# Kernel tuning notes

Hardware: AMD Instinct MI355X
Metric: run time of the kernel (lower is better)

The kernel has to match this reference:

```python
import jax, jax.numpy as jnp
import numpy as np

N_NODES = 80000
N_EDGES = 1280000
IN_CH = 128
OUT_CH = 32
HID = 2 * OUT_CH


def gcn_conv(x, W, b, src, dst, n_nodes):
    """PyG GCNConv with self-loops and symmetric normalization.
    out[i] = b + sum_{j->i} deg(j)^-1/2 deg(i)^-1/2 (x_j @ W)
    """
    loop = jnp.arange(n_nodes, dtype=src.dtype)
    s = jnp.concatenate([src, loop])  # [E+N]
    d = jnp.concatenate([dst, loop])  # [E+N]
    deg = jax.ops.segment_sum(jnp.ones_like(d, dtype=x.dtype), d,
                              num_segments=n_nodes)  # in-degree incl. self loop
    dinv = jnp.where(deg > 0, jax.lax.rsqrt(deg), 0.0)
    norm = dinv[s] * dinv[d]  # [E+N]
    h = x @ W  # [N, F_out] dense transform first (fewer flops when F_out < F_in)
    msg = h[s] * norm[:, None]  # [E+N, F_out] gather + scale
    out = jax.ops.segment_sum(msg, d, num_segments=n_nodes)  # scatter-add
    return out + b


def setup_inputs() -> dict:
    key = jax.random.key(0)
    k1, k2, k3, k4 = jax.random.split(key, 4)
    x = jax.random.normal(k1, (N_NODES, IN_CH), dtype=jnp.float32)
    edge_index = jax.random.randint(k2, (2, N_EDGES), 0, N_NODES, dtype=jnp.int64)
    W1 = jax.random.normal(k3, (IN_CH, HID), dtype=jnp.float32) / np.sqrt(IN_CH)
    b1 = jnp.zeros((HID,), dtype=jnp.float32)
    W2 = jax.random.normal(k4, (HID, OUT_CH), dtype=jnp.float32) / np.sqrt(HID)
    b2 = jnp.zeros((OUT_CH,), dtype=jnp.float32)
    return {"x": x, "edge_index": edge_index, "W1": W1, "b1": b1,
            "W2": W2, "b2": b2}


def reference(x, edge_index, W1, b1, W2, b2):
    src, dst = edge_index[0], edge_index[1]
    h = jax.nn.relu(gcn_conv(x, W1, b1, src, dst, N_NODES))
    return gcn_conv(h, W2, b2, src, dst, N_NODES)
```

## Files before the change

### kernel.cpp

```cpp
#include <hip/hip_runtime.h>
#include <hip/hip_fp16.h>

#define N_NODES 80000
#define N_EDGES 1280000
#define IN_CH 128
#define HID 64
#define OUT_CH 32

#define NBUCK 625
#define CAP 3072
#define BIN_BLOCKS 256

typedef float vf2 __attribute__((ext_vector_type(2)));
typedef float vf4 __attribute__((ext_vector_type(4)));
typedef short short8 __attribute__((ext_vector_type(8)));
typedef float floatx4 __attribute__((ext_vector_type(4)));

__device__ __forceinline__ unsigned bf16rn(float x) {
    unsigned u = __float_as_uint(x);
    return (u + 0x7FFFu + ((u >> 16) & 1u)) >> 16;
}
__device__ __forceinline__ unsigned packbf2(float a, float b) {
    return bf16rn(a) | (bf16rn(b) << 16);
}
__device__ __forceinline__ float hl(unsigned u) {
    return __half2float(__ushort_as_half((unsigned short)(u & 0xFFFFu)));
}
__device__ __forceinline__ float hh(unsigned u) {
    return __half2float(__ushort_as_half((unsigned short)(u >> 16)));
}
__device__ __forceinline__ unsigned pack2h(float a, float b) {
    return (unsigned)__half_as_ushort(__float2half_rn(a)) |
           ((unsigned)__half_as_ushort(__float2half_rn(b)) << 16);
}

__global__ __launch_bounds__(256) void k_bin_gemm1(
        const int* __restrict__ src, const int* __restrict__ dst,
        int* __restrict__ gcur, unsigned int* __restrict__ binned,
        const float* __restrict__ x, const float* __restrict__ W1,
        unsigned short* __restrict__ h1h) {
    __shared__ unsigned short smem_u[26112];
    int bid = blockIdx.x, t = threadIdx.x;
    if (bid < BIN_BLOCKS) {
        int* hist = (int*)smem_u;
        int* lcur = hist + NBUCK;
        const int chunk = N_EDGES / BIN_BLOCKS;
        int e0 = bid * chunk;
        int e1 = e0 + chunk;
        for (int i = t; i < NBUCK; i += 256) hist[i] = 0;
        __syncthreads();
        for (int e = e0 + t; e < e1; e += 256)
            atomicAdd(&hist[dst[e] >> 7], 1);
        __syncthreads();
        for (int i = t; i < NBUCK; i += 256) {
            int h = hist[i];
            lcur[i] = h ? atomicAdd(&gcur[i], h) : 0;
        }
        __syncthreads();
        for (int e = e0 + t; e < e1; e += 256) {
            int d = dst[e];
            int bk = d >> 7;
            int pos = atomicAdd(&lcur[bk], 1);
            if (pos < CAP)
                binned[(size_t)bk * CAP + pos] =
                    (unsigned int)src[e] | ((unsigned int)(d & 127) << 17);
        }
    } else {
        unsigned short* sX = smem_u;
        unsigned short* sWT = smem_u + 128 * 136;
        long long nb = (long long)(bid - BIN_BLOCKS) * 128;
        for (int it = 0; it < 16; ++it) {
            int idx = t + it * 256;
            int node = idx >> 5, k4 = (idx & 31) * 4;
            float4 v = *(const float4*)&x[(nb + node) * IN_CH + k4];
            unsigned u0 = packbf2(v.x, v.y), u1 = packbf2(v.z, v.w);
            *(uint2*)&sX[node * 136 + k4] = (uint2){u0, u1};
        }
        for (int it = 0; it < 8; ++it) {
            int idx = t + it * 256;
            int k = idx >> 4, c4 = (idx & 15) * 4;
            float4 w = *(const float4*)&W1[k * 64 + c4];
            sWT[(c4 + 0) * 136 + k] = (unsigned short)bf16rn(w.x);
            sWT[(c4 + 1) * 136 + k] = (unsigned short)bf16rn(w.y);
            sWT[(c4 + 2) * 136 + k] = (unsigned short)bf16rn(w.z);
            sWT[(c4 + 3) * 136 + k] = (unsigned short)bf16rn(w.w);
        }
        __syncthreads();
        int wv = t >> 6, lane = t & 63;
        int lm = lane & 15, q = lane >> 4;
        int m0 = wv * 32;
        floatx4 acc[2][4];
#pragma unroll
        for (int i = 0; i < 2; ++i)
#pragma unroll
            for (int j = 0; j < 4; ++j) acc[i][j] = (floatx4){0.f, 0.f, 0.f, 0.f};
#pragma unroll
        for (int kk = 0; kk < 128; kk += 32) {
            short8 a0 = *(short8*)&sX[(m0 + lm) * 136 + kk + q * 8];
            short8 a1 = *(short8*)&sX[(m0 + 16 + lm) * 136 + kk + q * 8];
#pragma unroll
            for (int ct = 0; ct < 4; ++ct) {
                short8 bfr = *(short8*)&sWT[(ct * 16 + lm) * 136 + kk + q * 8];
                acc[0][ct] = __builtin_amdgcn_mfma_f32_16x16x32_bf16(a0, bfr, acc[0][ct], 0, 0, 0);
                acc[1][ct] = __builtin_amdgcn_mfma_f32_16x16x32_bf16(a1, bfr, acc[1][ct], 0, 0, 0);
            }
        }
#pragma unroll
        for (int mt = 0; mt < 2; ++mt)
#pragma unroll
            for (int ct = 0; ct < 4; ++ct)
#pragma unroll
                for (int r = 0; r < 4; ++r) {
                    long long node = nb + m0 + mt * 16 + q * 4 + r;
                    int c = ct * 16 + lm;
                    h1h[node * 64 + c] = __half_as_ushort(__float2half_rn(acc[mt][ct][r]));
                }
    }
}

__global__ __launch_bounds__(256) void k_csr(const unsigned int* __restrict__ binned,
                                             const int* __restrict__ cnt,
                                             int* __restrict__ csr,
                                             int* __restrict__ rs, int* __restrict__ re,
                                             float* __restrict__ dinv) {
    __shared__ int deg[128];
    __shared__ int scan[128];
    __shared__ int cur[128];
    int bk = blockIdx.x, t = threadIdx.x;
    int n_e = min(cnt[bk], CAP);
    const unsigned int* eb = binned + (size_t)bk * CAP;
    if (t < 128) deg[t] = 0;
    __syncthreads();
    for (int i = t; i < n_e; i += 256) atomicAdd(&deg[eb[i] >> 17], 1);
    __syncthreads();
    if (t < 128) scan[t] = deg[t];
    __syncthreads();
    for (int off = 1; off < 128; off <<= 1) {
        int v = (t < 128 && t >= off) ? scan[t - off] : 0;
        __syncthreads();
        if (t < 128) scan[t] += v;
        __syncthreads();
    }
    if (t < 128) {
        int incl = scan[t];
        int s = incl - deg[t];
        cur[t] = s;
        int n = bk * 128 + t;
        int base = bk * CAP;
        rs[n] = base + s;
        re[n] = base + incl;
        dinv[n] = rsqrtf((float)(deg[t] + 1));
    }
    __syncthreads();
    for (int i = t; i < n_e; i += 256) {
        unsigned int p = eb[i];
        int dL = p >> 17;
        int pos = atomicAdd(&cur[dL], 1);
        csr[bk * CAP + pos] = (int)(p & 0x1FFFF);
    }
}

__global__ __launch_bounds__(256) void k_agg64(
        const unsigned int* __restrict__ h1u, const int* __restrict__ csr,
        const int* __restrict__ rs_, const int* __restrict__ re_,
        const float* __restrict__ dinv, const float* __restrict__ b1,
        float* __restrict__ h2) {
    int n = blockIdx.x * 4 + (threadIdx.x >> 6);
    int lane = threadIdx.x & 63;
    int half = lane >> 5, fo = lane & 31;
    int a = rs_[n], b = re_[n];
    float ax = 0.f, ay = 0.f;
    int e = a + half;
    for (; e + 6 < b; e += 8) {
        int s0 = csr[e], s1 = csr[e + 2], s2 = csr[e + 4], s3 = csr[e + 6];
        unsigned u0 = h1u[(size_t)s0 * 32 + fo]; float d0 = dinv[s0];
        unsigned u1 = h1u[(size_t)s1 * 32 + fo]; float d1 = dinv[s1];
        unsigned u2 = h1u[(size_t)s2 * 32 + fo]; float d2 = dinv[s2];
        unsigned u3 = h1u[(size_t)s3 * 32 + fo]; float d3 = dinv[s3];
        ax += d0 * hl(u0); ay += d0 * hh(u0);
        ax += d1 * hl(u1); ay += d1 * hh(u1);
        ax += d2 * hl(u2); ay += d2 * hh(u2);
        ax += d3 * hl(u3); ay += d3 * hh(u3);
    }
    for (; e < b; e += 2) {
        int s = csr[e];
        unsigned u = h1u[(size_t)s * 32 + fo];
        float d = dinv[s];
        ax += d * hl(u); ay += d * hh(u);
    }
    ax += __shfl_down(ax, 32);
    ay += __shfl_down(ay, 32);
    if (half == 0) {
        float dn = dinv[n];
        unsigned un = h1u[(size_t)n * 32 + fo];
        ax += dn * hl(un); ay += dn * hh(un);
        float2 bb = *(const float2*)&b1[2 * fo];
        float2 o = {fmaxf(dn * ax + bb.x, 0.f), fmaxf(dn * ay + bb.y, 0.f)};
        *(float2*)&h2[(size_t)n * 64 + 2 * fo] = o;
    }
}

__global__ __launch_bounds__(256) void k_gemm2(const float* __restrict__ h2,
                                               const float* __restrict__ W2,
                                               unsigned int* __restrict__ g2u) {
    __shared__ float sX[64 * 68];
    __shared__ float sW[64 * 32];
    int t = threadIdx.x;
    long long nb = (long long)blockIdx.x * 64;
    for (int i = t * 4; i < 64 * 32; i += 1024) {
        *(float4*)&sW[i] = *(const float4*)&W2[i];
    }
    for (int r = 0; r < 4; ++r) {
        int n = (t >> 4) + r * 16;
        int k4 = (t & 15) * 4;
        *(float4*)&sX[n * 68 + k4] = *(const float4*)&h2[(nb + n) * HID + k4];
    }
    __syncthreads();
    int tx = t & 7, ty = t >> 3;
    float acc0[4] = {0, 0, 0, 0}, acc1[4] = {0, 0, 0, 0};
#pragma unroll 4
    for (int k = 0; k < 64; ++k) {
        float4 w = *(float4*)&sW[k * 32 + tx * 4];
        float x0 = sX[(ty * 2 + 0) * 68 + k];
        float x1 = sX[(ty * 2 + 1) * 68 + k];
        acc0[0] += x0 * w.x; acc0[1] += x0 * w.y; acc0[2] += x0 * w.z; acc0[3] += x0 * w.w;
        acc1[0] += x1 * w.x; acc1[1] += x1 * w.y; acc1[2] += x1 * w.z; acc1[3] += x1 * w.w;
    }
    long long n = nb + ty * 2;
    uint2 p0 = {pack2h(acc0[0], acc0[1]), pack2h(acc0[2], acc0[3])};
    *(uint2*)&g2u[n * 16 + tx * 2] = p0;
    uint2 p1 = {pack2h(acc1[0], acc1[1]), pack2h(acc1[2], acc1[3])};
    *(uint2*)&g2u[(n + 1) * 16 + tx * 2] = p1;
}

__global__ __launch_bounds__(256) void k_agg32(
        const unsigned int* __restrict__ g2u, const int* __restrict__ csr,
        const int* __restrict__ rs_, const int* __restrict__ re_,
        const float* __restrict__ dinv, const float* __restrict__ b2,
        float* __restrict__ outp) {
    int n = blockIdx.x * 4 + (threadIdx.x >> 6);
    int lane = threadIdx.x & 63;
    int oc = lane >> 3, fo = lane & 7;
    int a = rs_[n], b = re_[n];
    float ax = 0.f, ay = 0.f, az = 0.f, aw = 0.f;
    int e = a + oc;
    for (; e + 8 < b; e += 16) {
        int s0 = csr[e], s1 = csr[e + 8];
        uint2 u0 = *(const uint2*)&g2u[(size_t)s0 * 16 + 2 * fo]; float d0 = dinv[s0];
        uint2 u1 = *(const uint2*)&g2u[(size_t)s1 * 16 + 2 * fo]; float d1 = dinv[s1];
        ax += d0 * hl(u0.x); ay += d0 * hh(u0.x);
        az += d0 * hl(u0.y); aw += d0 * hh(u0.y);
        ax += d1 * hl(u1.x); ay += d1 * hh(u1.x);
        az += d1 * hl(u1.y); aw += d1 * hh(u1.y);
    }
    for (; e < b; e += 8) {
        int s = csr[e];
        uint2 u = *(const uint2*)&g2u[(size_t)s * 16 + 2 * fo];
        float d = dinv[s];
        ax += d * hl(u.x); ay += d * hh(u.x);
        az += d * hl(u.y); aw += d * hh(u.y);
    }
    ax += __shfl_down(ax, 32); ay += __shfl_down(ay, 32);
    az += __shfl_down(az, 32); aw += __shfl_down(aw, 32);
    ax += __shfl_down(ax, 16); ay += __shfl_down(ay, 16);
    az += __shfl_down(az, 16); aw += __shfl_down(aw, 16);
    ax += __shfl_down(ax, 8);  ay += __shfl_down(ay, 8);
    az += __shfl_down(az, 8);  aw += __shfl_down(aw, 8);
    if (oc == 0) {
        float dn = dinv[n];
        uint2 un = *(const uint2*)&g2u[(size_t)n * 16 + 2 * fo];
        ax += dn * hl(un.x); ay += dn * hh(un.x);
        az += dn * hl(un.y); aw += dn * hh(un.y);
        float4 bb = *(const float4*)&b2[4 * fo];
        vf4 o = {dn * ax + bb.x, dn * ay + bb.y, dn * az + bb.z, dn * aw + bb.w};
        __builtin_nontemporal_store(o, (vf4*)&outp[(size_t)n * 32 + 4 * fo]);
    }
}

static inline size_t align256(size_t x) { return (x + 255) & ~(size_t)255; }

extern "C" void kernel_launch(void* const* d_in, const int* in_sizes, int n_in,
                              void* d_out, int out_size, void* d_ws, size_t ws_size,
                              hipStream_t stream) {
    const float* x  = (const float*)d_in[0];
    const int*   ei = (const int*)d_in[1];
    const float* W1 = (const float*)d_in[2];
    const float* b1 = (const float*)d_in[3];
    const float* W2 = (const float*)d_in[4];
    const float* b2 = (const float*)d_in[5];
    float* out = (float*)d_out;

    const int* src = ei;
    const int* dst = ei + N_EDGES;

    char* ws = (char*)d_ws;
    size_t off = 0;
    int* gcur = (int*)(ws + off);              off = align256(off + NBUCK * 4);
    unsigned int* binned = (unsigned int*)(ws + off);
                                               off = align256(off + (size_t)NBUCK * CAP * 4);
    int* csr = (int*)(ws + off);               off = align256(off + (size_t)NBUCK * CAP * 4);
    int* rs  = (int*)(ws + off);               off = align256(off + (size_t)N_NODES * 4);
    int* re  = (int*)(ws + off);               off = align256(off + (size_t)N_NODES * 4);
    float* dinv = (float*)(ws + off);          off = align256(off + (size_t)N_NODES * 4);
    unsigned short* h1h = (unsigned short*)(ws + off);
                                               off = align256(off + (size_t)N_NODES * 64 * 2);
    float* h2 = (float*)(ws + off);            off = align256(off + (size_t)N_NODES * HID * 4);
    unsigned int* g2u = (unsigned int*)h1h;

    (void)hipMemsetAsync(gcur, 0, NBUCK * 4, stream);
    k_bin_gemm1<<<BIN_BLOCKS + N_NODES / 128, 256, 0, stream>>>(src, dst, gcur, binned,
                                                                x, W1, h1h);
    k_csr<<<NBUCK, 256, 0, stream>>>(binned, gcur, csr, rs, re, dinv);
    k_agg64<<<N_NODES / 4, 256, 0, stream>>>((const unsigned int*)h1h, csr, rs, re,
                                             dinv, b1, h2);
    k_gemm2<<<N_NODES / 64, 256, 0, stream>>>(h2, W2, g2u);
    k_agg32<<<N_NODES / 4, 256, 0, stream>>>(g2u, csr, rs, re, dinv, b2, out);
}
```

Baseline: 219.2 us.

## Fuse layer-2 GEMM into layer-1 aggregation and shrink GEMM1 tiles

```diff
diff --git a/kernel.cpp b/kernel.cpp
--- a/kernel.cpp
+++ b/kernel.cpp
@@ -9,9 +9,8 @@
 
 #define NBUCK 625
 #define CAP 3072
-#define BIN_BLOCKS 256
-
-typedef float vf2 __attribute__((ext_vector_type(2)));
+#define BIN_BLOCKS 1024
+
 typedef float vf4 __attribute__((ext_vector_type(4)));
 typedef short short8 __attribute__((ext_vector_type(8)));
 typedef float floatx4 __attribute__((ext_vector_type(4)));
@@ -39,7 +38,7 @@
         int* __restrict__ gcur, unsigned int* __restrict__ binned,
         const float* __restrict__ x, const float* __restrict__ W1,
         unsigned short* __restrict__ h1h) {
-    __shared__ unsigned short smem_u[26112];
+    __shared__ unsigned short smem_u[17408];
     int bid = blockIdx.x, t = threadIdx.x;
     if (bid < BIN_BLOCKS) {
         int* hist = (int*)smem_u;
@@ -67,9 +66,9 @@
         }
     } else {
         unsigned short* sX = smem_u;
-        unsigned short* sWT = smem_u + 128 * 136;
-        long long nb = (long long)(bid - BIN_BLOCKS) * 128;
-        for (int it = 0; it < 16; ++it) {
+        unsigned short* sWT = smem_u + 64 * 136;
+        long long nb = (long long)(bid - BIN_BLOCKS) * 64;
+        for (int it = 0; it < 8; ++it) {
             int idx = t + it * 256;
             int node = idx >> 5, k4 = (idx & 31) * 4;
             float4 v = *(const float4*)&x[(nb + node) * IN_CH + k4];
@@ -88,33 +87,27 @@
         __syncthreads();
         int wv = t >> 6, lane = t & 63;
         int lm = lane & 15, q = lane >> 4;
-        int m0 = wv * 32;
-        floatx4 acc[2][4];
-#pragma unroll
-        for (int i = 0; i < 2; ++i)
-#pragma unroll
-            for (int j = 0; j < 4; ++j) acc[i][j] = (floatx4){0.f, 0.f, 0.f, 0.f};
+        int m0 = wv * 16;
+        floatx4 acc[4];
+#pragma unroll
+        for (int j = 0; j < 4; ++j) acc[j] = (floatx4){0.f, 0.f, 0.f, 0.f};
 #pragma unroll
         for (int kk = 0; kk < 128; kk += 32) {
-            short8 a0 = *(short8*)&sX[(m0 + lm) * 136 + kk + q * 8];
-            short8 a1 = *(short8*)&sX[(m0 + 16 + lm) * 136 + kk + q * 8];
+            short8 a = *(short8*)&sX[(m0 + lm) * 136 + kk + q * 8];
 #pragma unroll
             for (int ct = 0; ct < 4; ++ct) {
                 short8 bfr = *(short8*)&sWT[(ct * 16 + lm) * 136 + kk + q * 8];
-                acc[0][ct] = __builtin_amdgcn_mfma_f32_16x16x32_bf16(a0, bfr, acc[0][ct], 0, 0, 0);
-                acc[1][ct] = __builtin_amdgcn_mfma_f32_16x16x32_bf16(a1, bfr, acc[1][ct], 0, 0, 0);
+                acc[ct] = __builtin_amdgcn_mfma_f32_16x16x32_bf16(a, bfr, acc[ct], 0, 0, 0);
             }
         }
 #pragma unroll
-        for (int mt = 0; mt < 2; ++mt)
-#pragma unroll
-            for (int ct = 0; ct < 4; ++ct)
-#pragma unroll
-                for (int r = 0; r < 4; ++r) {
-                    long long node = nb + m0 + mt * 16 + q * 4 + r;
-                    int c = ct * 16 + lm;
-                    h1h[node * 64 + c] = __half_as_ushort(__float2half_rn(acc[mt][ct][r]));
-                }
+        for (int ct = 0; ct < 4; ++ct)
+#pragma unroll
+            for (int r = 0; r < 4; ++r) {
+                long long node = nb + m0 + q * 4 + r;
+                int c = ct * 16 + lm;
+                h1h[node * 64 + c] = __half_as_ushort(__float2half_rn(acc[ct][r]));
+            }
     }
 }
 
@@ -160,13 +153,20 @@
     }
 }
 
-__global__ __launch_bounds__(256) void k_agg64(
+__global__ __launch_bounds__(256) void k_agg64g2(
         const unsigned int* __restrict__ h1u, const int* __restrict__ csr,
         const int* __restrict__ rs_, const int* __restrict__ re_,
         const float* __restrict__ dinv, const float* __restrict__ b1,
-        float* __restrict__ h2) {
-    int n = blockIdx.x * 4 + (threadIdx.x >> 6);
-    int lane = threadIdx.x & 63;
+        const float* __restrict__ W2, unsigned int* __restrict__ g2u) {
+    __shared__ unsigned int sW2[32 * 32];
+    int t = threadIdx.x;
+    for (int i = t; i < 1024; i += 256) {
+        int j = i >> 5, c = i & 31;
+        sW2[i] = pack2h(W2[(2 * j) * 32 + c], W2[(2 * j + 1) * 32 + c]);
+    }
+    __syncthreads();
+    int wv = t >> 6, lane = t & 63;
+    int n = blockIdx.x * 4 + wv;
     int half = lane >> 5, fo = lane & 31;
     int a = rs_[n], b = re_[n];
     float ax = 0.f, ay = 0.f;
@@ -190,47 +190,27 @@
     }
     ax += __shfl_down(ax, 32);
     ay += __shfl_down(ay, 32);
-    if (half == 0) {
-        float dn = dinv[n];
-        unsigned un = h1u[(size_t)n * 32 + fo];
-        ax += dn * hl(un); ay += dn * hh(un);
-        float2 bb = *(const float2*)&b1[2 * fo];
-        float2 o = {fmaxf(dn * ax + bb.x, 0.f), fmaxf(dn * ay + bb.y, 0.f)};
-        *(float2*)&h2[(size_t)n * 64 + 2 * fo] = o;
-    }
-}
-
-__global__ __launch_bounds__(256) void k_gemm2(const float* __restrict__ h2,
-                                               const float* __restrict__ W2,
-                                               unsigned int* __restrict__ g2u) {
-    __shared__ float sX[64 * 68];
-    __shared__ float sW[64 * 32];
-    int t = threadIdx.x;
-    long long nb = (long long)blockIdx.x * 64;
-    for (int i = t * 4; i < 64 * 32; i += 1024) {
-        *(float4*)&sW[i] = *(const float4*)&W2[i];
-    }
-    for (int r = 0; r < 4; ++r) {
-        int n = (t >> 4) + r * 16;
-        int k4 = (t & 15) * 4;
-        *(float4*)&sX[n * 68 + k4] = *(const float4*)&h2[(nb + n) * HID + k4];
-    }
-    __syncthreads();
-    int tx = t & 7, ty = t >> 3;
-    float acc0[4] = {0, 0, 0, 0}, acc1[4] = {0, 0, 0, 0};
-#pragma unroll 4
-    for (int k = 0; k < 64; ++k) {
-        float4 w = *(float4*)&sW[k * 32 + tx * 4];
-        float x0 = sX[(ty * 2 + 0) * 68 + k];
-        float x1 = sX[(ty * 2 + 1) * 68 + k];
-        acc0[0] += x0 * w.x; acc0[1] += x0 * w.y; acc0[2] += x0 * w.z; acc0[3] += x0 * w.w;
-        acc1[0] += x1 * w.x; acc1[1] += x1 * w.y; acc1[2] += x1 * w.z; acc1[3] += x1 * w.w;
-    }
-    long long n = nb + ty * 2;
-    uint2 p0 = {pack2h(acc0[0], acc0[1]), pack2h(acc0[2], acc0[3])};
-    *(uint2*)&g2u[n * 16 + tx * 2] = p0;
-    uint2 p1 = {pack2h(acc1[0], acc1[1]), pack2h(acc1[2], acc1[3])};
-    *(uint2*)&g2u[(n + 1) * 16 + tx * 2] = p1;
+    float dn = dinv[n];
+    unsigned un = h1u[(size_t)n * 32 + fo];
+    ax += dn * hl(un); ay += dn * hh(un);
+    float2 bb = *(const float2*)&b1[2 * fo];
+    float hx = fmaxf(dn * ax + bb.x, 0.f);
+    float hy = fmaxf(dn * ay + bb.y, 0.f);
+    int jb = half * 16;
+    float sum = 0.f;
+#pragma unroll
+    for (int i = 0; i < 16; ++i) {
+        int j = jb + i;
+        float h0 = __shfl(hx, j);
+        float h1v = __shfl(hy, j);
+        unsigned w = sW2[j * 32 + fo];
+        sum += h0 * hl(w) + h1v * hh(w);
+    }
+    sum += __shfl_down(sum, 32);
+    float v0 = __shfl(sum, 2 * (lane & 15));
+    float v1 = __shfl(sum, 2 * (lane & 15) + 1);
+    if (lane < 16)
+        g2u[(size_t)n * 16 + lane] = pack2h(v0, v1);
 }
 
 __global__ __launch_bounds__(256) void k_agg32(
@@ -304,15 +284,14 @@
     float* dinv = (float*)(ws + off);          off = align256(off + (size_t)N_NODES * 4);
     unsigned short* h1h = (unsigned short*)(ws + off);
                                                off = align256(off + (size_t)N_NODES * 64 * 2);
-    float* h2 = (float*)(ws + off);            off = align256(off + (size_t)N_NODES * HID * 4);
-    unsigned int* g2u = (unsigned int*)h1h;
+    unsigned int* g2u = (unsigned int*)(ws + off);
+                                               off = align256(off + (size_t)N_NODES * 16 * 4);
 
     (void)hipMemsetAsync(gcur, 0, NBUCK * 4, stream);
-    k_bin_gemm1<<<BIN_BLOCKS + N_NODES / 128, 256, 0, stream>>>(src, dst, gcur, binned,
-                                                                x, W1, h1h);
+    k_bin_gemm1<<<BIN_BLOCKS + N_NODES / 64, 256, 0, stream>>>(src, dst, gcur, binned,
+                                                               x, W1, h1h);
     k_csr<<<NBUCK, 256, 0, stream>>>(binned, gcur, csr, rs, re, dinv);
-    k_agg64<<<N_NODES / 4, 256, 0, stream>>>((const unsigned int*)h1h, csr, rs, re,
-                                             dinv, b1, h2);
-    k_gemm2<<<N_NODES / 64, 256, 0, stream>>>(h2, W2, g2u);
+    k_agg64g2<<<N_NODES / 4, 256, 0, stream>>>((const unsigned int*)h1h, csr, rs, re,
+                                               dinv, b1, W2, g2u);
     k_agg32<<<N_NODES / 4, 256, 0, stream>>>(g2u, csr, rs, re, dinv, b2, out);
 }
```

New measurement: 245.4 us. +12.0%, slower.
